# Optimization experiments

Measured on AMD Instinct MI355X. Metric: run time of the kernel, lower is better.

## Reference

```python
import jax, jax.numpy as jnp
import numpy as np

D = 768          # n_embd
I = 3072         # moe_intermediate_size (4 * n_embd)
E = 8            # n_routed_experts
K = 2            # num_experts_per_tok
LIMIT = 10.0     # swiglu_limit
VOCAB = 32768


def setup_inputs() -> dict:
    key = jax.random.key(0)
    ks = jax.random.split(key, 10)
    s = 0.02
    return {
        "x": jax.random.normal(ks[0], (1, 2048, D), dtype=jnp.float32),
        "input_ids": jax.random.randint(ks[1], (1, 2048), 0, VOCAB, dtype=jnp.int64),
        "gate_w": jax.random.normal(ks[2], (D, E), dtype=jnp.float32) * s,
        "gate_bias": jnp.zeros((E,), dtype=jnp.float32),
        "w1": jax.random.normal(ks[3], (E, D, I), dtype=jnp.float32) * s,
        "w2": jax.random.normal(ks[4], (E, I, D), dtype=jnp.float32) * s,
        "w3": jax.random.normal(ks[5], (E, D, I), dtype=jnp.float32) * s,
        "w1s": jax.random.normal(ks[6], (D, I), dtype=jnp.float32) * s,
        "w2s": jax.random.normal(ks[7], (I, D), dtype=jnp.float32) * s,
        "w3s": jax.random.normal(ks[8], (D, I), dtype=jnp.float32) * s,
    }


def _expert(xf, W1, W2, W3):
    # SwiGLU with asymmetric clamping, as in DeepSeekExpert (swiglu_limit > 0)
    gate = jnp.minimum(xf @ W1, LIMIT)               # clamp max only
    up = jnp.clip(xf @ W3, -LIMIT, LIMIT)            # clamp both sides
    return (jax.nn.silu(gate) * up) @ W2


def reference(x, input_ids, gate_w, gate_bias, w1, w2, w3, w1s, w2s, w3s):
    B, T, _ = x.shape
    flat = x.reshape(-1, D)                           # [N, D], N = B*T
    N = flat.shape[0]

    # gating: sqrtsoftplus scoring
    scores = jnp.sqrt(jax.nn.softplus(flat @ gate_w))  # [N, E]
    routed_scores = scores + gate_bias                 # gate_bias used only for topk selection
    _, indices = jax.lax.top_k(routed_scores, K)       # [N, K]

    weights = jnp.take_along_axis(scores, indices, axis=1)  # [N, K]
    # norm_topk_prob=True; routed_scaling_factor=1.0
    weights = weights / jnp.clip(weights.sum(axis=-1, keepdims=True), 1e-6)

    # dense combine matrix [N, E] (jit-friendly dispatch/combine)
    combine = jnp.zeros((N, E), dtype=weights.dtype)
    combine = combine.at[jnp.arange(N)[:, None], indices].add(weights)

    # shared expert on all tokens
    y = _expert(flat, w1s, w2s, w3s)                   # [N, D]

    # routed experts: batched grouped GEMM over all tokens, then weighted combine
    gate_h = jnp.minimum(jnp.einsum('td,edi->eti', flat, w1), LIMIT)   # [E, N, I]
    up_h = jnp.clip(jnp.einsum('td,edi->eti', flat, w3), -LIMIT, LIMIT)
    h = jax.nn.silu(gate_h) * up_h                     # [E, N, I]
    out_e = jnp.einsum('eti,eid->etd', h, w2)          # [E, N, D]
    routed = jnp.einsum('etd,te->td', out_e, combine)  # [N, D]

    return (y + routed).reshape(B, T, D)
```

## Files before the change

### kernel.cpp

```cpp
#include <hip/hip_runtime.h>


#define D_ 768
#define I_ 3072
#define E_ 8
#define NTOK 2048
#define NPMAX 5120
#define MAXTILES 40
#define NSHT 16
#define SPLITK 4
#define KS_ (I_ / SPLITK)

typedef __bf16 bf16x8 __attribute__((ext_vector_type(8)));
typedef float floatx4 __attribute__((ext_vector_type(4)));

#define GLOAD_LDS16(g, l) __builtin_amdgcn_global_load_lds( \
    (const __attribute__((address_space(1))) void*)(g),     \
    (__attribute__((address_space(3))) void*)(l), 16, 0, 0)

__device__ __forceinline__ unsigned short f2b(float f) {
    unsigned int u = __float_as_uint(f);
    u += 0x7fffu + ((u >> 16) & 1u);
    return (unsigned short)(u >> 16);
}
__device__ __forceinline__ float b2f(unsigned short u) {
    return __uint_as_float((unsigned int)u << 16);
}


__global__ __launch_bounds__(256) void prep_kernel(
    const float* __restrict__ x, const float* __restrict__ gw,
    const float* __restrict__ gbias,
    const float* __restrict__ w1, const float* __restrict__ w2,
    const float* __restrict__ w3, const float* __restrict__ w1s,
    const float* __restrict__ w2s, const float* __restrict__ w3s,
    unsigned short* __restrict__ xb,
    unsigned short* __restrict__ w1b, unsigned short* __restrict__ w3b,
    unsigned short* __restrict__ w2b, unsigned short* __restrict__ w1sb,
    unsigned short* __restrict__ w3sb, unsigned short* __restrict__ w2sb,
    int* __restrict__ idx, float* __restrict__ wts) {
    __shared__ float t[64][65];
    int b = blockIdx.x, tid = threadIdx.x;
    if (b < 15552) {
        const float* s; unsigned short* d; int R, C, bx, by;
        if (b < 10368) {
            int z = b / 576, r = b % 576; bx = r % 48; by = r / 48; R = D_; C = I_;
            if (z < 8)       { s = w1 + (size_t)z * D_ * I_;       d = w1b + (size_t)z * D_ * I_; }
            else if (z < 16) { s = w3 + (size_t)(z - 8) * D_ * I_; d = w3b + (size_t)(z - 8) * D_ * I_; }
            else if (z == 16){ s = w1s; d = w1sb; }
            else             { s = w3s; d = w3sb; }
        } else {
            int bb = b - 10368;
            int z = bb / 576, r = bb % 576; bx = r % 12; by = r / 12; R = I_; C = D_;
            if (z < 8) { s = w2 + (size_t)z * I_ * D_; d = w2b + (size_t)z * I_ * D_; }
            else       { s = w2s; d = w2sb; }
        }
        int c0 = bx * 64, r0 = by * 64;
#pragma unroll
        for (int j = 0; j < 4; j++) {
            int slot = tid + j * 256;
            int rr = slot >> 4, c4 = (slot & 15) * 4;
            float4 v = *(const float4*)(s + (size_t)(r0 + rr) * C + c0 + c4);
            t[rr][c4] = v.x; t[rr][c4 + 1] = v.y; t[rr][c4 + 2] = v.z; t[rr][c4 + 3] = v.w;
        }
        __syncthreads();
#pragma unroll
        for (int j = 0; j < 2; j++) {
            int slot = tid + j * 256;
            int c = slot >> 3, rs = (slot & 7) * 8;
            unsigned short o[8] __attribute__((aligned(16)));
#pragma unroll
            for (int i = 0; i < 8; i++) o[i] = f2b(t[rs + i][c]);
            *(int4*)(d + (size_t)(c0 + c) * R + r0 + rs) = *(const int4*)o;
        }
    } else if (b < 17088) {
        int gid = (b - 15552) * 256 + tid;
        float4 v = *(const float4*)(x + (size_t)gid * 4);
        ushort4 o;
        o.x = f2b(v.x); o.y = f2b(v.y); o.z = f2b(v.z); o.w = f2b(v.w);
        *(ushort4*)(xb + (size_t)gid * 4) = o;
    } else {
        int tok = (b - 17088) * 4 + (tid >> 6);
        int lane = tid & 63;
        float z[E_];
#pragma unroll
        for (int e = 0; e < E_; e++) z[e] = 0.f;
        const float* xr = x + (size_t)tok * D_;
        for (int j = lane; j < D_; j += 64) {
            float xv = xr[j];
            const float* g = gw + (size_t)j * E_;
#pragma unroll
            for (int e = 0; e < E_; e++) z[e] += xv * g[e];
        }
#pragma unroll
        for (int off = 32; off > 0; off >>= 1)
#pragma unroll
            for (int e = 0; e < E_; e++) z[e] += __shfl_down(z[e], off, 64);
        if (lane == 0) {
            float s[E_], r[E_];
#pragma unroll
            for (int e = 0; e < E_; e++) {
                float zz = z[e];
                float sp = zz > 0.f ? zz + log1pf(expf(-zz)) : log1pf(expf(zz));
                s[e] = sqrtf(sp);
                r[e] = s[e] + gbias[e];
            }
            int i0 = 0;
            for (int e = 1; e < E_; e++) if (r[e] > r[i0]) i0 = e;
            int i1 = (i0 == 0) ? 1 : 0;
            for (int e = 0; e < E_; e++) if (e != i0 && r[e] > r[i1]) i1 = e;
            float w0 = s[i0], w1v = s[i1];
            float inv = 1.f / fmaxf(w0 + w1v, 1e-6f);
            idx[2 * tok] = i0; idx[2 * tok + 1] = i1;
            wts[2 * tok] = w0 * inv; wts[2 * tok + 1] = w1v * inv;
        }
    }
}


__global__ void route_build_kernel(const int* __restrict__ idx,
                                   const float* __restrict__ wts,
                                   int* __restrict__ pair_token,
                                   float* __restrict__ pair_w,
                                   int* __restrict__ pos_of,
                                   int* __restrict__ tiles) {
    __shared__ int cnt[E_], seg[E_], cur[E_];
    int tid = threadIdx.x;
    if (tid < E_) { cnt[tid] = 0; cur[tid] = 0; }
    __syncthreads();
    for (int p = tid; p < NTOK * 2; p += 256) atomicAdd(&cnt[idx[p]], 1);
    __syncthreads();
    if (tid == 0) {
        int off = 0, nt = 0;
        for (int e = 0; e < E_; e++) {
            seg[e] = off;
            int te = (cnt[e] + 127) >> 7;
            for (int j = 0; j < te; j++) {
                tiles[nt * 2] = e; tiles[nt * 2 + 1] = off + j * 128; nt++;
            }
            off += te * 128;
        }
        for (; nt < MAXTILES; nt++) { tiles[nt * 2] = -1; tiles[nt * 2 + 1] = 0; }
    }
    for (int p = tid; p < NPMAX; p += 256) pair_token[p] = -1;
    __syncthreads();
    for (int p = tid; p < NTOK * 2; p += 256) {
        int e = idx[p];
        int r = atomicAdd(&cur[e], 1);
        int pos = seg[e] + r;
        pair_token[pos] = p >> 1;
        pair_w[pos] = wts[p];
        pos_of[p] = pos;
    }
}


__launch_bounds__(256)
__global__ void gemm_act_kernel(const unsigned short* __restrict__ xb,
                                const unsigned short* __restrict__ w1sb,
                                const unsigned short* __restrict__ w3sb,
                                const unsigned short* __restrict__ w1b,
                                const unsigned short* __restrict__ w3b,
                                const int* __restrict__ tiles,
                                const int* __restrict__ pair_token,
                                unsigned short* __restrict__ act_s,
                                unsigned short* __restrict__ act_r) {
    __shared__ __align__(16) unsigned short As[128 * 32];
    __shared__ __align__(16) unsigned short Bs1[128 * 32];
    __shared__ __align__(16) unsigned short Bs3[128 * 32];

    int mt = blockIdx.y;
    const unsigned short *B1, *B3;
    unsigned short* C;
    int m0; bool routed;
    if (mt < NSHT) {
        B1 = w1sb; B3 = w3sb; C = act_s; m0 = mt * 128; routed = false;
    } else {
        int e = tiles[(mt - NSHT) * 2];
        if (e < 0) return;
        m0 = tiles[(mt - NSHT) * 2 + 1];
        B1 = w1b + (size_t)e * I_ * D_; B3 = w3b + (size_t)e * I_ * D_;
        C = act_r; routed = true;
    }
    int n0 = blockIdx.x * 128;
    int tid = threadIdx.x;
    int lane = tid & 63, wave = tid >> 6;
    int wm = (wave & 1) * 64, wn = (wave >> 1) * 64;
    int l15 = lane & 15, quad = lane >> 4;

    int r = tid >> 2;
    int lc8 = (((tid & 3) ^ ((r >> 1) & 3)) * 8);
    int tokA0, tokA1;
    if (routed) {
        tokA0 = pair_token[m0 + r];      if (tokA0 < 0) tokA0 = 0;
        tokA1 = pair_token[m0 + r + 64]; if (tokA1 < 0) tokA1 = 0;
    } else { tokA0 = m0 + r; tokA1 = m0 + r + 64; }
    const unsigned short* ApA0 = xb + (size_t)tokA0 * D_ + lc8;
    const unsigned short* ApA1 = xb + (size_t)tokA1 * D_ + lc8;
    const unsigned short* B1p0 = B1 + (size_t)(n0 + r) * D_ + lc8;
    const unsigned short* B1p1 = B1 + (size_t)(n0 + r + 64) * D_ + lc8;
    const unsigned short* B3p0 = B3 + (size_t)(n0 + r) * D_ + lc8;
    const unsigned short* B3p1 = B3 + (size_t)(n0 + r + 64) * D_ + lc8;
    unsigned short* lA0  = As  + wave * 512;
    unsigned short* lA1  = As  + 2048 + wave * 512;
    unsigned short* lB10 = Bs1 + wave * 512;
    unsigned short* lB11 = Bs1 + 2048 + wave * 512;
    unsigned short* lB30 = Bs3 + wave * 512;
    unsigned short* lB31 = Bs3 + 2048 + wave * 512;

    int swz = (quad ^ ((l15 >> 1) & 3)) * 8;
    floatx4 acc1[4][4] = {}; floatx4 acc3[4][4] = {};

    for (int k0 = 0; k0 < D_; k0 += 32) {
        __syncthreads();
        GLOAD_LDS16(ApA0 + k0, lA0);
        GLOAD_LDS16(ApA1 + k0, lA1);
        GLOAD_LDS16(B1p0 + k0, lB10);
        GLOAD_LDS16(B1p1 + k0, lB11);
        GLOAD_LDS16(B3p0 + k0, lB30);
        GLOAD_LDS16(B3p1 + k0, lB31);
        __syncthreads();

        bf16x8 af[4], b1f[4], b3f[4];
#pragma unroll
        for (int mi = 0; mi < 4; mi++)
            af[mi] = *(const bf16x8*)(As + (wm + mi * 16 + l15) * 32 + swz);
#pragma unroll
        for (int ni = 0; ni < 4; ni++) {
            b1f[ni] = *(const bf16x8*)(Bs1 + (wn + ni * 16 + l15) * 32 + swz);
            b3f[ni] = *(const bf16x8*)(Bs3 + (wn + ni * 16 + l15) * 32 + swz);
        }
#pragma unroll
        for (int mi = 0; mi < 4; mi++)
#pragma unroll
            for (int ni = 0; ni < 4; ni++) {
                acc1[mi][ni] = __builtin_amdgcn_mfma_f32_16x16x32_bf16(
                    af[mi], b1f[ni], acc1[mi][ni], 0, 0, 0);
                acc3[mi][ni] = __builtin_amdgcn_mfma_f32_16x16x32_bf16(
                    af[mi], b3f[ni], acc3[mi][ni], 0, 0, 0);
            }
    }

#pragma unroll
    for (int mi = 0; mi < 4; mi++)
#pragma unroll
        for (int ni = 0; ni < 4; ni++) {
            int col = n0 + wn + ni * 16 + l15;
#pragma unroll
            for (int rr = 0; rr < 4; rr++) {
                int row = m0 + wm + mi * 16 + quad * 4 + rr;
                float g = fminf(acc1[mi][ni][rr], 10.f);
                float u = fminf(fmaxf(acc3[mi][ni][rr], -10.f), 10.f);
                float a = g / (1.f + __expf(-g)) * u;
                C[(size_t)row * I_ + col] = f2b(a);
            }
        }
}


__launch_bounds__(256)
__global__ void gemm_out_kernel(const unsigned short* __restrict__ act_s,
                                const unsigned short* __restrict__ act_r,
                                const unsigned short* __restrict__ w2sb,
                                const unsigned short* __restrict__ w2b,
                                const int* __restrict__ tiles,
                                unsigned short* __restrict__ ysp,
                                unsigned short* __restrict__ rop) {
    __shared__ __align__(16) unsigned short As[128 * 32];
    __shared__ __align__(16) unsigned short Bs[128 * 32];

    int mt = blockIdx.y, ks = blockIdx.z;
    int kbase = ks * KS_;
    const unsigned short *A, *B;
    unsigned short* C;
    int m0;
    if (mt < NSHT) {
        A = act_s; B = w2sb; C = ysp + (size_t)ks * NTOK * D_; m0 = mt * 128;
    } else {
        int e = tiles[(mt - NSHT) * 2];
        if (e < 0) return;
        m0 = tiles[(mt - NSHT) * 2 + 1];
        A = act_r; B = w2b + (size_t)e * I_ * D_; C = rop + (size_t)ks * NPMAX * D_;
    }
    int n0 = blockIdx.x * 128;
    int tid = threadIdx.x;
    int lane = tid & 63, wave = tid >> 6;
    int wm = (wave & 1) * 64, wn = (wave >> 1) * 64;
    int l15 = lane & 15, quad = lane >> 4;

    int r = tid >> 2;
    int lc8 = (((tid & 3) ^ ((r >> 1) & 3)) * 8);
    const unsigned short* Ap0 = A + (size_t)(m0 + r) * I_ + kbase + lc8;
    const unsigned short* Ap1 = A + (size_t)(m0 + r + 64) * I_ + kbase + lc8;
    const unsigned short* Bp0 = B + (size_t)(n0 + r) * I_ + kbase + lc8;
    const unsigned short* Bp1 = B + (size_t)(n0 + r + 64) * I_ + kbase + lc8;
    unsigned short* lA0 = As + wave * 512;
    unsigned short* lA1 = As + 2048 + wave * 512;
    unsigned short* lB0 = Bs + wave * 512;
    unsigned short* lB1 = Bs + 2048 + wave * 512;

    int swz = (quad ^ ((l15 >> 1) & 3)) * 8;
    floatx4 acc[4][4] = {};

    for (int k0 = 0; k0 < KS_; k0 += 32) {
        __syncthreads();
        GLOAD_LDS16(Ap0 + k0, lA0);
        GLOAD_LDS16(Ap1 + k0, lA1);
        GLOAD_LDS16(Bp0 + k0, lB0);
        GLOAD_LDS16(Bp1 + k0, lB1);
        __syncthreads();

        bf16x8 af[4], bf[4];
#pragma unroll
        for (int mi = 0; mi < 4; mi++)
            af[mi] = *(const bf16x8*)(As + (wm + mi * 16 + l15) * 32 + swz);
#pragma unroll
        for (int ni = 0; ni < 4; ni++)
            bf[ni] = *(const bf16x8*)(Bs + (wn + ni * 16 + l15) * 32 + swz);
#pragma unroll
        for (int mi = 0; mi < 4; mi++)
#pragma unroll
            for (int ni = 0; ni < 4; ni++)
                acc[mi][ni] = __builtin_amdgcn_mfma_f32_16x16x32_bf16(
                    af[mi], bf[ni], acc[mi][ni], 0, 0, 0);
    }

#pragma unroll
    for (int mi = 0; mi < 4; mi++)
#pragma unroll
        for (int ni = 0; ni < 4; ni++) {
            int col = n0 + wn + ni * 16 + l15;
#pragma unroll
            for (int rr = 0; rr < 4; rr++) {
                int row = m0 + wm + mi * 16 + quad * 4 + rr;
                C[(size_t)row * D_ + col] = f2b(acc[mi][ni][rr]);
            }
        }
}


__global__ void combine_kernel(const unsigned short* __restrict__ ysp,
                               const unsigned short* __restrict__ rop,
                               const int* __restrict__ pos_of,
                               const float* __restrict__ pair_w,
                               float* __restrict__ out) {
    int gid = blockIdx.x * 256 + threadIdx.x;
    int t = gid / (D_ / 4);
    int j = (gid % (D_ / 4)) * 4;
    int p0 = pos_of[2 * t], p1 = pos_of[2 * t + 1];
    float w0 = pair_w[p0], w1 = pair_w[p1];
    float a0 = 0.f, a1 = 0.f, a2 = 0.f, a3 = 0.f;
#pragma unroll
    for (int ks = 0; ks < SPLITK; ks++) {
        ushort4 a = *(const ushort4*)(ysp + ((size_t)ks * NTOK + t) * D_ + j);
        ushort4 b = *(const ushort4*)(rop + ((size_t)ks * NPMAX + p0) * D_ + j);
        ushort4 c = *(const ushort4*)(rop + ((size_t)ks * NPMAX + p1) * D_ + j);
        a0 += b2f(a.x) + w0 * b2f(b.x) + w1 * b2f(c.x);
        a1 += b2f(a.y) + w0 * b2f(b.y) + w1 * b2f(c.y);
        a2 += b2f(a.z) + w0 * b2f(b.z) + w1 * b2f(c.z);
        a3 += b2f(a.w) + w0 * b2f(b.w) + w1 * b2f(c.w);
    }
    float4 o; o.x = a0; o.y = a1; o.z = a2; o.w = a3;
    *(float4*)(out + (size_t)t * D_ + j) = o;
}


extern "C" void kernel_launch(void* const* d_in, const int* in_sizes, int n_in,
                              void* d_out, int out_size, void* d_ws, size_t ws_size,
                              hipStream_t stream) {
    (void)in_sizes; (void)n_in; (void)out_size; (void)ws_size;
    const float* x   = (const float*)d_in[0];
    const float* gw  = (const float*)d_in[2];
    const float* gb  = (const float*)d_in[3];
    const float* w1  = (const float*)d_in[4];
    const float* w2  = (const float*)d_in[5];
    const float* w3  = (const float*)d_in[6];
    const float* w1s = (const float*)d_in[7];
    const float* w2s = (const float*)d_in[8];
    const float* w3s = (const float*)d_in[9];
    float* out = (float*)d_out;

    char* ws = (char*)d_ws;
    size_t off = 0;
    auto alloc = [&](size_t bytes) {
        size_t o = (off + 255) & ~(size_t)255;
        off = o + bytes;
        return (void*)(ws + o);
    };
    unsigned short* xb   = (unsigned short*)alloc((size_t)NTOK * D_ * 2);
    unsigned short* w1b  = (unsigned short*)alloc((size_t)E_ * I_ * D_ * 2);
    unsigned short* w3b  = (unsigned short*)alloc((size_t)E_ * I_ * D_ * 2);
    unsigned short* w2b  = (unsigned short*)alloc((size_t)E_ * I_ * D_ * 2);
    unsigned short* w1sb = (unsigned short*)alloc((size_t)I_ * D_ * 2);
    unsigned short* w3sb = (unsigned short*)alloc((size_t)I_ * D_ * 2);
    unsigned short* w2sb = (unsigned short*)alloc((size_t)I_ * D_ * 2);
    unsigned short* acts = (unsigned short*)alloc((size_t)NTOK * I_ * 2);
    unsigned short* actr = (unsigned short*)alloc((size_t)NPMAX * I_ * 2);
    unsigned short* ysp  = (unsigned short*)alloc((size_t)SPLITK * NTOK * D_ * 2);
    unsigned short* rop  = (unsigned short*)alloc((size_t)SPLITK * NPMAX * D_ * 2);
    int*   idx  = (int*)alloc((size_t)NTOK * 2 * 4);
    float* wts  = (float*)alloc((size_t)NTOK * 2 * 4);
    int*   ptok = (int*)alloc((size_t)NPMAX * 4);
    float* pw   = (float*)alloc((size_t)NPMAX * 4);
    int*   posf = (int*)alloc((size_t)NTOK * 2 * 4);
    int*   tls  = (int*)alloc((size_t)MAXTILES * 2 * 4);

    prep_kernel<<<17600, 256, 0, stream>>>(x, gw, gb, w1, w2, w3, w1s, w2s, w3s,
                                           xb, w1b, w3b, w2b, w1sb, w3sb, w2sb,
                                           idx, wts);
    route_build_kernel<<<1, 256, 0, stream>>>(idx, wts, ptok, pw, posf, tls);
    gemm_act_kernel<<<dim3(I_ / 128, NSHT + MAXTILES), 256, 0, stream>>>(
        xb, w1sb, w3sb, w1b, w3b, tls, ptok, acts, actr);
    gemm_out_kernel<<<dim3(D_ / 128, NSHT + MAXTILES, SPLITK), 256, 0, stream>>>(
        acts, actr, w2sb, w2b, tls, ysp, rop);
    combine_kernel<<<NTOK * (D_ / 4) / 256, 256, 0, stream>>>(ysp, rop, posf, pw, out);
}
```

Measured before the change: 522.7 us.

## Retile MoE GEMMs to 128x64 with BK=64, merge buffers, fp32 split-K partials

Both expert GEMM kernels change from 128x128 tiles with a K step of 32 to 128x64 tiles with a K step of 64, using a new XOR swizzle in LDS. This doubles the block count and halves the number of barrier pairs per K. Shared and routed activations now live in one unified buffer. Split-K for the output GEMM drops from 4 to 2, and partials are stored in fp32 instead of bf16. This removes a rounding step but doubles the bytes per partial that the combine kernel reads.

Measured after the change: 467.1 us. 1.12x faster.

```diff
diff --git a/kernel.cpp b/kernel.cpp
--- a/kernel.cpp
+++ b/kernel.cpp
@@ -8,7 +8,8 @@
 #define NPMAX 5120
 #define MAXTILES 40
 #define NSHT 16
-#define SPLITK 4
+#define ROWS (NTOK + NPMAX)
+#define SPLITK 2
 #define KS_ (I_ / SPLITK)
 
 typedef __bf16 bf16x8 __attribute__((ext_vector_type(8)));
@@ -22,9 +23,6 @@
     unsigned int u = __float_as_uint(f);
     u += 0x7fffu + ((u >> 16) & 1u);
     return (unsigned short)(u >> 16);
-}
-__device__ __forceinline__ float b2f(unsigned short u) {
-    return __uint_as_float((unsigned int)u << 16);
 }
 
 
@@ -163,88 +161,99 @@
                                 const unsigned short* __restrict__ w3b,
                                 const int* __restrict__ tiles,
                                 const int* __restrict__ pair_token,
-                                unsigned short* __restrict__ act_s,
-                                unsigned short* __restrict__ act_r) {
-    __shared__ __align__(16) unsigned short As[128 * 32];
-    __shared__ __align__(16) unsigned short Bs1[128 * 32];
-    __shared__ __align__(16) unsigned short Bs3[128 * 32];
+                                unsigned short* __restrict__ act) {
+    __shared__ __align__(16) unsigned short As[128 * 64];
+    __shared__ __align__(16) unsigned short Bs1[64 * 64];
+    __shared__ __align__(16) unsigned short Bs3[64 * 64];
 
     int mt = blockIdx.y;
     const unsigned short *B1, *B3;
-    unsigned short* C;
     int m0; bool routed;
     if (mt < NSHT) {
-        B1 = w1sb; B3 = w3sb; C = act_s; m0 = mt * 128; routed = false;
+        B1 = w1sb; B3 = w3sb; m0 = mt * 128; routed = false;
     } else {
         int e = tiles[(mt - NSHT) * 2];
         if (e < 0) return;
-        m0 = tiles[(mt - NSHT) * 2 + 1];
+        m0 = NTOK + tiles[(mt - NSHT) * 2 + 1];
         B1 = w1b + (size_t)e * I_ * D_; B3 = w3b + (size_t)e * I_ * D_;
-        C = act_r; routed = true;
-    }
-    int n0 = blockIdx.x * 128;
+        routed = true;
+    }
+    int n0 = blockIdx.x * 64;
     int tid = threadIdx.x;
     int lane = tid & 63, wave = tid >> 6;
-    int wm = (wave & 1) * 64, wn = (wave >> 1) * 64;
+    int wm = (wave & 1) * 64, wn = (wave >> 1) * 32;
     int l15 = lane & 15, quad = lane >> 4;
 
-    int r = tid >> 2;
-    int lc8 = (((tid & 3) ^ ((r >> 1) & 3)) * 8);
-    int tokA0, tokA1;
-    if (routed) {
-        tokA0 = pair_token[m0 + r];      if (tokA0 < 0) tokA0 = 0;
-        tokA1 = pair_token[m0 + r + 64]; if (tokA1 < 0) tokA1 = 0;
-    } else { tokA0 = m0 + r; tokA1 = m0 + r + 64; }
-    const unsigned short* ApA0 = xb + (size_t)tokA0 * D_ + lc8;
-    const unsigned short* ApA1 = xb + (size_t)tokA1 * D_ + lc8;
-    const unsigned short* B1p0 = B1 + (size_t)(n0 + r) * D_ + lc8;
-    const unsigned short* B1p1 = B1 + (size_t)(n0 + r + 64) * D_ + lc8;
-    const unsigned short* B3p0 = B3 + (size_t)(n0 + r) * D_ + lc8;
-    const unsigned short* B3p1 = B3 + (size_t)(n0 + r + 64) * D_ + lc8;
-    unsigned short* lA0  = As  + wave * 512;
-    unsigned short* lA1  = As  + 2048 + wave * 512;
-    unsigned short* lB10 = Bs1 + wave * 512;
-    unsigned short* lB11 = Bs1 + 2048 + wave * 512;
-    unsigned short* lB30 = Bs3 + wave * 512;
-    unsigned short* lB31 = Bs3 + 2048 + wave * 512;
-
-    int swz = (quad ^ ((l15 >> 1) & 3)) * 8;
-    floatx4 acc1[4][4] = {}; floatx4 acc3[4][4] = {};
-
-    for (int k0 = 0; k0 < D_; k0 += 32) {
+    int rl = lane >> 3;
+    int ph = lane & 7;
+    int lg = ph ^ rl;
+    const unsigned short* asrc[4];
+#pragma unroll
+    for (int j = 0; j < 4; j++) {
+        int r = j * 32 + wave * 8 + rl;
+        int tok;
+        if (routed) { tok = pair_token[m0 - NTOK + r]; if (tok < 0) tok = 0; }
+        else tok = m0 + r;
+        asrc[j] = xb + (size_t)tok * D_ + lg * 8;
+    }
+    const unsigned short *b1src[2], *b3src[2];
+#pragma unroll
+    for (int j = 0; j < 2; j++) {
+        int r = j * 32 + wave * 8 + rl;
+        b1src[j] = B1 + (size_t)(n0 + r) * D_ + lg * 8;
+        b3src[j] = B3 + (size_t)(n0 + r) * D_ + lg * 8;
+    }
+    unsigned short *ldA[4], *ldB1[2], *ldB3[2];
+#pragma unroll
+    for (int j = 0; j < 4; j++) ldA[j] = As + (j * 32 + wave * 8) * 64;
+#pragma unroll
+    for (int j = 0; j < 2; j++) {
+        ldB1[j] = Bs1 + (j * 32 + wave * 8) * 64;
+        ldB3[j] = Bs3 + (j * 32 + wave * 8) * 64;
+    }
+
+    floatx4 acc1[4][2] = {}; floatx4 acc3[4][2] = {};
+    int sx = (l15 & 7);
+
+    for (int k0 = 0; k0 < D_; k0 += 64) {
         __syncthreads();
-        GLOAD_LDS16(ApA0 + k0, lA0);
-        GLOAD_LDS16(ApA1 + k0, lA1);
-        GLOAD_LDS16(B1p0 + k0, lB10);
-        GLOAD_LDS16(B1p1 + k0, lB11);
-        GLOAD_LDS16(B3p0 + k0, lB30);
-        GLOAD_LDS16(B3p1 + k0, lB31);
+#pragma unroll
+        for (int j = 0; j < 4; j++) GLOAD_LDS16(asrc[j] + k0, ldA[j]);
+#pragma unroll
+        for (int j = 0; j < 2; j++) {
+            GLOAD_LDS16(b1src[j] + k0, ldB1[j]);
+            GLOAD_LDS16(b3src[j] + k0, ldB3[j]);
+        }
         __syncthreads();
 
-        bf16x8 af[4], b1f[4], b3f[4];
-#pragma unroll
-        for (int mi = 0; mi < 4; mi++)
-            af[mi] = *(const bf16x8*)(As + (wm + mi * 16 + l15) * 32 + swz);
-#pragma unroll
-        for (int ni = 0; ni < 4; ni++) {
-            b1f[ni] = *(const bf16x8*)(Bs1 + (wn + ni * 16 + l15) * 32 + swz);
-            b3f[ni] = *(const bf16x8*)(Bs3 + (wn + ni * 16 + l15) * 32 + swz);
-        }
-#pragma unroll
-        for (int mi = 0; mi < 4; mi++)
-#pragma unroll
-            for (int ni = 0; ni < 4; ni++) {
-                acc1[mi][ni] = __builtin_amdgcn_mfma_f32_16x16x32_bf16(
-                    af[mi], b1f[ni], acc1[mi][ni], 0, 0, 0);
-                acc3[mi][ni] = __builtin_amdgcn_mfma_f32_16x16x32_bf16(
-                    af[mi], b3f[ni], acc3[mi][ni], 0, 0, 0);
+#pragma unroll
+        for (int kk = 0; kk < 2; kk++) {
+            int pq = ((kk * 4 + quad) ^ sx) * 8;
+            bf16x8 af[4], b1f[2], b3f[2];
+#pragma unroll
+            for (int mi = 0; mi < 4; mi++)
+                af[mi] = *(const bf16x8*)(As + (wm + mi * 16 + l15) * 64 + pq);
+#pragma unroll
+            for (int ni = 0; ni < 2; ni++) {
+                b1f[ni] = *(const bf16x8*)(Bs1 + (wn + ni * 16 + l15) * 64 + pq);
+                b3f[ni] = *(const bf16x8*)(Bs3 + (wn + ni * 16 + l15) * 64 + pq);
             }
+#pragma unroll
+            for (int mi = 0; mi < 4; mi++)
+#pragma unroll
+                for (int ni = 0; ni < 2; ni++) {
+                    acc1[mi][ni] = __builtin_amdgcn_mfma_f32_16x16x32_bf16(
+                        af[mi], b1f[ni], acc1[mi][ni], 0, 0, 0);
+                    acc3[mi][ni] = __builtin_amdgcn_mfma_f32_16x16x32_bf16(
+                        af[mi], b3f[ni], acc3[mi][ni], 0, 0, 0);
+                }
+        }
     }
 
 #pragma unroll
     for (int mi = 0; mi < 4; mi++)
 #pragma unroll
-        for (int ni = 0; ni < 4; ni++) {
+        for (int ni = 0; ni < 2; ni++) {
             int col = n0 + wn + ni * 16 + l15;
 #pragma unroll
             for (int rr = 0; rr < 4; rr++) {
@@ -252,95 +261,100 @@
                 float g = fminf(acc1[mi][ni][rr], 10.f);
                 float u = fminf(fmaxf(acc3[mi][ni][rr], -10.f), 10.f);
                 float a = g / (1.f + __expf(-g)) * u;
-                C[(size_t)row * I_ + col] = f2b(a);
+                act[(size_t)row * I_ + col] = f2b(a);
             }
         }
 }
 
 
 __launch_bounds__(256)
-__global__ void gemm_out_kernel(const unsigned short* __restrict__ act_s,
-                                const unsigned short* __restrict__ act_r,
+__global__ void gemm_out_kernel(const unsigned short* __restrict__ act,
                                 const unsigned short* __restrict__ w2sb,
                                 const unsigned short* __restrict__ w2b,
                                 const int* __restrict__ tiles,
-                                unsigned short* __restrict__ ysp,
-                                unsigned short* __restrict__ rop) {
-    __shared__ __align__(16) unsigned short As[128 * 32];
-    __shared__ __align__(16) unsigned short Bs[128 * 32];
+                                float* __restrict__ outp) {
+    __shared__ __align__(16) unsigned short As[128 * 64];
+    __shared__ __align__(16) unsigned short Bs[64 * 64];
 
     int mt = blockIdx.y, ks = blockIdx.z;
     int kbase = ks * KS_;
-    const unsigned short *A, *B;
-    unsigned short* C;
+    const unsigned short* B;
     int m0;
     if (mt < NSHT) {
-        A = act_s; B = w2sb; C = ysp + (size_t)ks * NTOK * D_; m0 = mt * 128;
+        B = w2sb; m0 = mt * 128;
     } else {
         int e = tiles[(mt - NSHT) * 2];
         if (e < 0) return;
-        m0 = tiles[(mt - NSHT) * 2 + 1];
-        A = act_r; B = w2b + (size_t)e * I_ * D_; C = rop + (size_t)ks * NPMAX * D_;
-    }
-    int n0 = blockIdx.x * 128;
+        m0 = NTOK + tiles[(mt - NSHT) * 2 + 1];
+        B = w2b + (size_t)e * I_ * D_;
+    }
+    float* C = outp + (size_t)ks * ROWS * D_;
+    int n0 = blockIdx.x * 64;
     int tid = threadIdx.x;
     int lane = tid & 63, wave = tid >> 6;
-    int wm = (wave & 1) * 64, wn = (wave >> 1) * 64;
+    int wm = (wave & 1) * 64, wn = (wave >> 1) * 32;
     int l15 = lane & 15, quad = lane >> 4;
 
-    int r = tid >> 2;
-    int lc8 = (((tid & 3) ^ ((r >> 1) & 3)) * 8);
-    const unsigned short* Ap0 = A + (size_t)(m0 + r) * I_ + kbase + lc8;
-    const unsigned short* Ap1 = A + (size_t)(m0 + r + 64) * I_ + kbase + lc8;
-    const unsigned short* Bp0 = B + (size_t)(n0 + r) * I_ + kbase + lc8;
-    const unsigned short* Bp1 = B + (size_t)(n0 + r + 64) * I_ + kbase + lc8;
-    unsigned short* lA0 = As + wave * 512;
-    unsigned short* lA1 = As + 2048 + wave * 512;
-    unsigned short* lB0 = Bs + wave * 512;
-    unsigned short* lB1 = Bs + 2048 + wave * 512;
-
-    int swz = (quad ^ ((l15 >> 1) & 3)) * 8;
-    floatx4 acc[4][4] = {};
-
-    for (int k0 = 0; k0 < KS_; k0 += 32) {
+    int rl = lane >> 3, ph = lane & 7, lg = ph ^ rl;
+    const unsigned short* asrc[4];
+#pragma unroll
+    for (int j = 0; j < 4; j++)
+        asrc[j] = act + (size_t)(m0 + j * 32 + wave * 8 + rl) * I_ + kbase + lg * 8;
+    const unsigned short* bsrc[2];
+#pragma unroll
+    for (int j = 0; j < 2; j++)
+        bsrc[j] = B + (size_t)(n0 + j * 32 + wave * 8 + rl) * I_ + kbase + lg * 8;
+    unsigned short *ldA[4], *ldB[2];
+#pragma unroll
+    for (int j = 0; j < 4; j++) ldA[j] = As + (j * 32 + wave * 8) * 64;
+#pragma unroll
+    for (int j = 0; j < 2; j++) ldB[j] = Bs + (j * 32 + wave * 8) * 64;
+
+    floatx4 acc[4][2] = {};
+    int sx = (l15 & 7);
+
+    for (int k0 = 0; k0 < KS_; k0 += 64) {
         __syncthreads();
-        GLOAD_LDS16(Ap0 + k0, lA0);
-        GLOAD_LDS16(Ap1 + k0, lA1);
-        GLOAD_LDS16(Bp0 + k0, lB0);
-        GLOAD_LDS16(Bp1 + k0, lB1);
+#pragma unroll
+        for (int j = 0; j < 4; j++) GLOAD_LDS16(asrc[j] + k0, ldA[j]);
+#pragma unroll
+        for (int j = 0; j < 2; j++) GLOAD_LDS16(bsrc[j] + k0, ldB[j]);
         __syncthreads();
 
-        bf16x8 af[4], bf[4];
-#pragma unroll
-        for (int mi = 0; mi < 4; mi++)
-            af[mi] = *(const bf16x8*)(As + (wm + mi * 16 + l15) * 32 + swz);
-#pragma unroll
-        for (int ni = 0; ni < 4; ni++)
-            bf[ni] = *(const bf16x8*)(Bs + (wn + ni * 16 + l15) * 32 + swz);
-#pragma unroll
-        for (int mi = 0; mi < 4; mi++)
-#pragma unroll
-            for (int ni = 0; ni < 4; ni++)
-                acc[mi][ni] = __builtin_amdgcn_mfma_f32_16x16x32_bf16(
-                    af[mi], bf[ni], acc[mi][ni], 0, 0, 0);
+#pragma unroll
+        for (int kk = 0; kk < 2; kk++) {
+            int pq = ((kk * 4 + quad) ^ sx) * 8;
+            bf16x8 af[4], bf[2];
+#pragma unroll
+            for (int mi = 0; mi < 4; mi++)
+                af[mi] = *(const bf16x8*)(As + (wm + mi * 16 + l15) * 64 + pq);
+#pragma unroll
+            for (int ni = 0; ni < 2; ni++)
+                bf[ni] = *(const bf16x8*)(Bs + (wn + ni * 16 + l15) * 64 + pq);
+#pragma unroll
+            for (int mi = 0; mi < 4; mi++)
+#pragma unroll
+                for (int ni = 0; ni < 2; ni++)
+                    acc[mi][ni] = __builtin_amdgcn_mfma_f32_16x16x32_bf16(
+                        af[mi], bf[ni], acc[mi][ni], 0, 0, 0);
+        }
     }
 
 #pragma unroll
     for (int mi = 0; mi < 4; mi++)
 #pragma unroll
-        for (int ni = 0; ni < 4; ni++) {
+        for (int ni = 0; ni < 2; ni++) {
             int col = n0 + wn + ni * 16 + l15;
 #pragma unroll
             for (int rr = 0; rr < 4; rr++) {
                 int row = m0 + wm + mi * 16 + quad * 4 + rr;
-                C[(size_t)row * D_ + col] = f2b(acc[mi][ni][rr]);
+                C[(size_t)row * D_ + col] = acc[mi][ni][rr];
             }
         }
 }
 
 
-__global__ void combine_kernel(const unsigned short* __restrict__ ysp,
-                               const unsigned short* __restrict__ rop,
+__global__ void combine_kernel(const float* __restrict__ outp,
                                const int* __restrict__ pos_of,
                                const float* __restrict__ pair_w,
                                float* __restrict__ out) {
@@ -352,13 +366,14 @@
     float a0 = 0.f, a1 = 0.f, a2 = 0.f, a3 = 0.f;
 #pragma unroll
     for (int ks = 0; ks < SPLITK; ks++) {
-        ushort4 a = *(const ushort4*)(ysp + ((size_t)ks * NTOK + t) * D_ + j);
-        ushort4 b = *(const ushort4*)(rop + ((size_t)ks * NPMAX + p0) * D_ + j);
-        ushort4 c = *(const ushort4*)(rop + ((size_t)ks * NPMAX + p1) * D_ + j);
-        a0 += b2f(a.x) + w0 * b2f(b.x) + w1 * b2f(c.x);
-        a1 += b2f(a.y) + w0 * b2f(b.y) + w1 * b2f(c.y);
-        a2 += b2f(a.z) + w0 * b2f(b.z) + w1 * b2f(c.z);
-        a3 += b2f(a.w) + w0 * b2f(b.w) + w1 * b2f(c.w);
+        const float* P = outp + (size_t)ks * ROWS * D_;
+        float4 a = *(const float4*)(P + (size_t)t * D_ + j);
+        float4 b = *(const float4*)(P + (size_t)(NTOK + p0) * D_ + j);
+        float4 c = *(const float4*)(P + (size_t)(NTOK + p1) * D_ + j);
+        a0 += a.x + w0 * b.x + w1 * c.x;
+        a1 += a.y + w0 * b.y + w1 * c.y;
+        a2 += a.z + w0 * b.z + w1 * c.z;
+        a3 += a.w + w0 * b.w + w1 * c.w;
     }
     float4 o; o.x = a0; o.y = a1; o.z = a2; o.w = a3;
     *(float4*)(out + (size_t)t * D_ + j) = o;
@@ -394,10 +409,8 @@
     unsigned short* w1sb = (unsigned short*)alloc((size_t)I_ * D_ * 2);
     unsigned short* w3sb = (unsigned short*)alloc((size_t)I_ * D_ * 2);
     unsigned short* w2sb = (unsigned short*)alloc((size_t)I_ * D_ * 2);
-    unsigned short* acts = (unsigned short*)alloc((size_t)NTOK * I_ * 2);
-    unsigned short* actr = (unsigned short*)alloc((size_t)NPMAX * I_ * 2);
-    unsigned short* ysp  = (unsigned short*)alloc((size_t)SPLITK * NTOK * D_ * 2);
-    unsigned short* rop  = (unsigned short*)alloc((size_t)SPLITK * NPMAX * D_ * 2);
+    unsigned short* act  = (unsigned short*)alloc((size_t)ROWS * I_ * 2);
+    float* outp = (float*)alloc((size_t)SPLITK * ROWS * D_ * 4);
     int*   idx  = (int*)alloc((size_t)NTOK * 2 * 4);
     float* wts  = (float*)alloc((size_t)NTOK * 2 * 4);
     int*   ptok = (int*)alloc((size_t)NPMAX * 4);
@@ -409,9 +422,9 @@
                                            xb, w1b, w3b, w2b, w1sb, w3sb, w2sb,
                                            idx, wts);
     route_build_kernel<<<1, 256, 0, stream>>>(idx, wts, ptok, pw, posf, tls);
-    gemm_act_kernel<<<dim3(I_ / 128, NSHT + MAXTILES), 256, 0, stream>>>(
-        xb, w1sb, w3sb, w1b, w3b, tls, ptok, acts, actr);
-    gemm_out_kernel<<<dim3(D_ / 128, NSHT + MAXTILES, SPLITK), 256, 0, stream>>>(
-        acts, actr, w2sb, w2b, tls, ysp, rop);
-    combine_kernel<<<NTOK * (D_ / 4) / 256, 256, 0, stream>>>(ysp, rop, posf, pw, out);
-}
+    gemm_act_kernel<<<dim3(I_ / 64, NSHT + MAXTILES), 256, 0, stream>>>(
+        xb, w1sb, w3sb, w1b, w3b, tls, ptok, act);
+    gemm_out_kernel<<<dim3(D_ / 64, NSHT + MAXTILES, SPLITK), 256, 0, stream>>>(
+        act, w2sb, w2b, tls, outp);
+    combine_kernel<<<NTOK * (D_ / 4) / 256, 256, 0, stream>>>(outp, posf, pw, out);
+}
```
